# Kernel optimization log

Hardware: AMD Instinct MI355X
Metric: run time of the kernel (lower is better)

The kernel has to match this reference:

```python
import jax, jax.numpy as jnp
import numpy as np

N, H, C = 65536, 256, 512  # tokens, hidden_dim, cond_dim


def setup_inputs() -> dict:
    key = jax.random.key(0)
    ks = jax.random.split(key, 8)
    s_h = 1.0 / np.sqrt(H)
    s_c = 1.0 / np.sqrt(C)
    return {
        "x": jax.random.normal(ks[0], (N, H), dtype=jnp.float32),
        "cond": jax.random.normal(ks[1], (N, C), dtype=jnp.float32),
        # FiLM: Linear(cond_dim -> 2*hidden_dim), output split into (gamma, beta)
        "W_film": jax.random.uniform(ks[2], (C, 2 * H), jnp.float32, -s_c, s_c),
        "b_film": jax.random.uniform(ks[3], (2 * H,), jnp.float32, -s_c, s_c),
        "W1": jax.random.uniform(ks[4], (H, H), jnp.float32, -s_h, s_h),
        "b1": jax.random.uniform(ks[5], (H,), jnp.float32, -s_h, s_h),
        "W2": jax.random.uniform(ks[6], (H, H), jnp.float32, -s_h, s_h),
        "b2": jax.random.uniform(ks[7], (H,), jnp.float32, -s_h, s_h),
    }


def reference(x, cond, W_film, b_film, W1, b1, W2, b2):
    # FiLM conditioning: gamma * x + beta (cond path; LayerNorm branch unused)
    gb = cond @ W_film + b_film            # [N, 2H]
    gamma, beta = gb[:, :H], gb[:, H:]
    h = gamma * x + beta
    # Dropout is identity in eval mode.
    h = jax.nn.relu(h) @ W1 + b1           # [N, H]
    h = jax.nn.relu(h) @ W2 + b2           # [N, H]
    return h + x                            # residual
```

## Files before the change

### kernel.cpp

```cpp
#include <hip/hip_runtime.h>
#include <hip/hip_bf16.h>


typedef __attribute__((ext_vector_type(8))) short bf16x8;
typedef __attribute__((ext_vector_type(4))) float f32x4;

typedef unsigned short ushort_t;
typedef unsigned int uint_t;

__device__ __forceinline__ ushort_t f2bf(float f) {
  union { float f; uint_t u; } v; v.f = f;
  uint_t u = v.u;
  return (ushort_t)((u + 0x7FFFu + ((u >> 16) & 1u)) >> 16);
}
__device__ __forceinline__ float bf2f(ushort_t s) {
  union { uint_t u; float f; } v; v.u = ((uint_t)s) << 16;
  return v.f;
}
__device__ __forceinline__ bf16x8 ldfrag(const ushort_t* p) {
  return *reinterpret_cast<const bf16x8*>(p);
}

__global__ void pack_weights(const float* __restrict__ Wf,
                             const float* __restrict__ W1,
                             const float* __restrict__ W2,
                             ushort_t* __restrict__ p1,
                             ushort_t* __restrict__ pW1,
                             ushort_t* __restrict__ pW2) {
  int u = blockIdx.x * 256 + threadIdx.x;
  if (u < 32768) {
    int lane = u & 63, rest = u >> 6;
    int kt = rest & 15;
    int kb = kt * 32 + (lane >> 4) * 8;
    int col = (rest >> 4) * 16 + (lane & 15);
#pragma unroll
    for (int j = 0; j < 8; ++j)
      p1[(size_t)u * 8 + j] = f2bf(Wf[(size_t)(kb + j) * 512 + col]);
  } else if (u < 40960) {
    int v = u - 32768;
    int lane = v & 63;
    int kt = (v >> 6) & 7;
    int kb = kt * 32 + (lane >> 4) * 8;
    int col = (v >> 9) * 16 + (lane & 15);
#pragma unroll
    for (int j = 0; j < 8; ++j)
      pW1[(size_t)v * 8 + j] = f2bf(W1[(size_t)(kb + j) * 256 + col]);
  } else if (u < 49152) {
    int v = u - 40960;
    int lane = v & 63;
    int kt = (v >> 6) & 7;
    int kb = kt * 32 + (lane >> 4) * 8;
    int col = (v >> 9) * 16 + (lane & 15);
#pragma unroll
    for (int j = 0; j < 8; ++j)
      pW2[(size_t)v * 8 + j] = f2bf(W2[(size_t)(kb + j) * 256 + col]);
  }
}

__global__ __launch_bounds__(256, 2)
void film_fused(const float* __restrict__ x, const float* __restrict__ cond,
                const float* __restrict__ b_film, const float* __restrict__ b1,
                const float* __restrict__ b2,
                const ushort_t* __restrict__ p1, const ushort_t* __restrict__ pW1,
                const ushort_t* __restrict__ pW2, float* __restrict__ out) {
  __shared__ __align__(16) char lds[65536];
  char* hbuf = lds;
  char* xbuf = lds + 32768;
  const int r0 = blockIdx.x * 64;
  const int t = threadIdx.x;
  const int w = t >> 6;
  const int l = t & 63;
  const int l15 = l & 15;
  const int lhi = l >> 4;

#pragma unroll
  for (int it = 0; it < 8; ++it) {
    int u = it * 256 + t;
    int row = u >> 5, k8 = u & 31;
    const float4* cs = reinterpret_cast<const float4*>(cond + (size_t)(r0 + row) * 512 + k8 * 8);
    float4 a = cs[0], b = cs[1];
    const float4* xs = reinterpret_cast<const float4*>(x + (size_t)(r0 + row) * 256 + k8 * 8);
    float4 xa = xs[0], xb = xs[1];
    int byte = row * 512 + k8 * 16;
    byte ^= ((row & 15) << 4);
    union { bf16x8 v; ushort_t s[8]; } hc;
    hc.s[0]=f2bf(a.x); hc.s[1]=f2bf(a.y); hc.s[2]=f2bf(a.z); hc.s[3]=f2bf(a.w);
    hc.s[4]=f2bf(b.x); hc.s[5]=f2bf(b.y); hc.s[6]=f2bf(b.z); hc.s[7]=f2bf(b.w);
    *reinterpret_cast<bf16x8*>(hbuf + byte) = hc.v;
    union { bf16x8 v; ushort_t s[8]; } hx;
    hx.s[0]=f2bf(xa.x); hx.s[1]=f2bf(xa.y); hx.s[2]=f2bf(xa.z); hx.s[3]=f2bf(xa.w);
    hx.s[4]=f2bf(xb.x); hx.s[5]=f2bf(xb.y); hx.s[6]=f2bf(xb.z); hx.s[7]=f2bf(xb.w);
    *reinterpret_cast<bf16x8*>(xbuf + byte) = hx.v;
  }

  bf16x8 bb[2][8];
#pragma unroll
  for (int tt = 0; tt < 8; ++tt) {
    int nt = (tt < 4) ? (w * 4 + tt) : (16 + w * 4 + (tt - 4));
    bb[0][tt] = ldfrag(p1 + ((nt * 16 + 0) * 64 + l) * 8);
  }
  __syncthreads();

  f32x4 acc1[4][8];
#pragma unroll
  for (int m = 0; m < 4; ++m)
#pragma unroll
    for (int n = 0; n < 8; ++n) acc1[m][n] = (f32x4){0.f, 0.f, 0.f, 0.f};

#pragma unroll
  for (int ktg = 0; ktg < 16; ++ktg) {
    if (ktg == 8) {
      __syncthreads();
#pragma unroll
      for (int it = 0; it < 8; ++it) {
        int u = it * 256 + t;
        int row = u >> 5, k8 = u & 31;
        const float4* cs = reinterpret_cast<const float4*>(cond + (size_t)(r0 + row) * 512 + 256 + k8 * 8);
        float4 a = cs[0], b = cs[1];
        int byte = row * 512 + k8 * 16;
        byte ^= ((row & 15) << 4);
        union { bf16x8 v; ushort_t s[8]; } hc;
        hc.s[0]=f2bf(a.x); hc.s[1]=f2bf(a.y); hc.s[2]=f2bf(a.z); hc.s[3]=f2bf(a.w);
        hc.s[4]=f2bf(b.x); hc.s[5]=f2bf(b.y); hc.s[6]=f2bf(b.z); hc.s[7]=f2bf(b.w);
        *reinterpret_cast<bf16x8*>(hbuf + byte) = hc.v;
      }
      __syncthreads();
    }
    const int cur = ktg & 1;
    if (ktg < 15) {
#pragma unroll
      for (int tt = 0; tt < 8; ++tt) {
        int nt = (tt < 4) ? (w * 4 + tt) : (16 + w * 4 + (tt - 4));
        bb[cur ^ 1][tt] = ldfrag(p1 + ((nt * 16 + (ktg + 1)) * 64 + l) * 8);
      }
    }
    bf16x8 afr[4];
    int ktl = ktg & 7;
#pragma unroll
    for (int m = 0; m < 4; ++m) {
      int row = m * 16 + l15;
      int byte = row * 512 + ktl * 64 + lhi * 16;
      byte ^= ((row & 15) << 4);
      afr[m] = *reinterpret_cast<const bf16x8*>(hbuf + byte);
    }
#pragma unroll
    for (int tt = 0; tt < 8; ++tt)
#pragma unroll
      for (int m = 0; m < 4; ++m)
        acc1[m][tt] = __builtin_amdgcn_mfma_f32_16x16x32_bf16(afr[m], bb[cur][tt], acc1[m][tt], 0, 0, 0);
  }
  __syncthreads();

#pragma unroll
  for (int tt = 0; tt < 4; ++tt) {
    int colg = w * 64 + tt * 16 + l15;
    float bg = b_film[colg];
    float bbv = b_film[256 + colg];
#pragma unroll
    for (int m = 0; m < 4; ++m) {
#pragma unroll
      for (int reg = 0; reg < 4; ++reg) {
        int row = m * 16 + lhi * 4 + reg;
        int byte = row * 512 + colg * 2;
        byte ^= ((row & 15) << 4);
        float xv = bf2f(*reinterpret_cast<const ushort_t*>(xbuf + byte));
        float h = fmaxf((acc1[m][tt][reg] + bg) * xv + (acc1[m][4 + tt][reg] + bbv), 0.f);
        *reinterpret_cast<ushort_t*>(hbuf + byte) = f2bf(h);
      }
    }
  }
  bf16x8 bb2[2][4];
#pragma unroll
  for (int tt = 0; tt < 4; ++tt) {
    int nt = w * 4 + tt;
    bb2[0][tt] = ldfrag(pW1 + ((nt * 8 + 0) * 64 + l) * 8);
  }
  __syncthreads();

  f32x4 acc2[4][4];
#pragma unroll
  for (int m = 0; m < 4; ++m)
#pragma unroll
    for (int n = 0; n < 4; ++n) acc2[m][n] = (f32x4){0.f, 0.f, 0.f, 0.f};

#pragma unroll
  for (int kt = 0; kt < 8; ++kt) {
    const int cur = kt & 1;
    if (kt < 7) {
#pragma unroll
      for (int tt = 0; tt < 4; ++tt) {
        int nt = w * 4 + tt;
        bb2[cur ^ 1][tt] = ldfrag(pW1 + ((nt * 8 + (kt + 1)) * 64 + l) * 8);
      }
    }
    bf16x8 afr[4];
#pragma unroll
    for (int m = 0; m < 4; ++m) {
      int row = m * 16 + l15;
      int byte = row * 512 + kt * 64 + lhi * 16;
      byte ^= ((row & 15) << 4);
      afr[m] = *reinterpret_cast<const bf16x8*>(hbuf + byte);
    }
#pragma unroll
    for (int tt = 0; tt < 4; ++tt)
#pragma unroll
      for (int m = 0; m < 4; ++m)
        acc2[m][tt] = __builtin_amdgcn_mfma_f32_16x16x32_bf16(afr[m], bb2[cur][tt], acc2[m][tt], 0, 0, 0);
  }
  __syncthreads();

#pragma unroll
  for (int tt = 0; tt < 4; ++tt) {
    int colg = w * 64 + tt * 16 + l15;
    float bias = b1[colg];
#pragma unroll
    for (int m = 0; m < 4; ++m) {
#pragma unroll
      for (int reg = 0; reg < 4; ++reg) {
        int row = m * 16 + lhi * 4 + reg;
        int byte = row * 512 + colg * 2;
        byte ^= ((row & 15) << 4);
        *reinterpret_cast<ushort_t*>(hbuf + byte) = f2bf(fmaxf(acc2[m][tt][reg] + bias, 0.f));
      }
    }
  }
  bf16x8 bb3[2][4];
#pragma unroll
  for (int tt = 0; tt < 4; ++tt) {
    int nt = w * 4 + tt;
    bb3[0][tt] = ldfrag(pW2 + ((nt * 8 + 0) * 64 + l) * 8);
  }
  __syncthreads();

  f32x4 acc3[4][4];
#pragma unroll
  for (int m = 0; m < 4; ++m)
#pragma unroll
    for (int n = 0; n < 4; ++n) acc3[m][n] = (f32x4){0.f, 0.f, 0.f, 0.f};

#pragma unroll
  for (int kt = 0; kt < 8; ++kt) {
    const int cur = kt & 1;
    if (kt < 7) {
#pragma unroll
      for (int tt = 0; tt < 4; ++tt) {
        int nt = w * 4 + tt;
        bb3[cur ^ 1][tt] = ldfrag(pW2 + ((nt * 8 + (kt + 1)) * 64 + l) * 8);
      }
    }
    bf16x8 afr[4];
#pragma unroll
    for (int m = 0; m < 4; ++m) {
      int row = m * 16 + l15;
      int byte = row * 512 + kt * 64 + lhi * 16;
      byte ^= ((row & 15) << 4);
      afr[m] = *reinterpret_cast<const bf16x8*>(hbuf + byte);
    }
#pragma unroll
    for (int tt = 0; tt < 4; ++tt)
#pragma unroll
      for (int m = 0; m < 4; ++m)
        acc3[m][tt] = __builtin_amdgcn_mfma_f32_16x16x32_bf16(afr[m], bb3[cur][tt], acc3[m][tt], 0, 0, 0);
  }
  __syncthreads();

  float b2v[4];
#pragma unroll
  for (int tt = 0; tt < 4; ++tt) b2v[tt] = b2[w * 64 + tt * 16 + l15];

#pragma unroll
  for (int h = 0; h < 2; ++h) {
#pragma unroll
    for (int tt = 0; tt < 4; ++tt) {
      int colg = w * 64 + tt * 16 + l15;
#pragma unroll
      for (int mm = 0; mm < 2; ++mm) {
        int m = h * 2 + mm;
#pragma unroll
        for (int reg = 0; reg < 4; ++reg) {
          int r = mm * 16 + lhi * 4 + reg;
          int byte = r * 1024 + colg * 4;
          byte ^= ((r & 15) << 4);
          *reinterpret_cast<float*>(hbuf + byte) = acc3[m][tt][reg] + b2v[tt];
        }
      }
    }
    __syncthreads();
#pragma unroll
    for (int i = 0; i < 8; ++i) {
      int u = i * 256 + t;
      int r = u >> 6, c4 = u & 63;
      int byte = r * 1024 + c4 * 16;
      byte ^= ((r & 15) << 4);
      f32x4 v = *reinterpret_cast<const f32x4*>(hbuf + byte);
      int grow = h * 32 + r;
      int xbyte = grow * 512 + c4 * 8;
      xbyte ^= ((grow & 15) << 4);
      const ushort_t* xp = reinterpret_cast<const ushort_t*>(xbuf + xbyte);
      v.x += bf2f(xp[0]); v.y += bf2f(xp[1]); v.z += bf2f(xp[2]); v.w += bf2f(xp[3]);
      f32x4* op = reinterpret_cast<f32x4*>(out + (size_t)(r0 + grow) * 256 + c4 * 4);
      __builtin_nontemporal_store(v, op);
    }
    if (h == 0) __syncthreads();
  }
}

extern "C" void kernel_launch(void* const* d_in, const int* in_sizes, int n_in,
                              void* d_out, int out_size, void* d_ws, size_t ws_size,
                              hipStream_t stream) {
  const float* x      = (const float*)d_in[0];
  const float* cond   = (const float*)d_in[1];
  const float* W_film = (const float*)d_in[2];
  const float* b_film = (const float*)d_in[3];
  const float* W1     = (const float*)d_in[4];
  const float* b1     = (const float*)d_in[5];
  const float* W2     = (const float*)d_in[6];
  const float* b2     = (const float*)d_in[7];
  float* out = (float*)d_out;

  ushort_t* p1  = (ushort_t*)d_ws;
  ushort_t* pW1 = p1 + 262144;
  ushort_t* pW2 = pW1 + 65536;

  hipLaunchKernelGGL(pack_weights, dim3(192), dim3(256), 0, stream,
                     W_film, W1, W2, p1, pW1, pW2);
  hipLaunchKernelGGL(film_fused, dim3(65536 / 64), dim3(256), 0, stream,
                     x, cond, b_film, b1, b2, p1, pW1, pW2, out);
}
```

Before: 108.0 us.

## Load full cond tile upfront, read x from global, double-buffer hidden activations in LDS

Stages the whole 64x512 bf16 cond tile into LDS at once, so the mid-GEMM reload and its two barriers go away. x is no longer kept as bf16 in LDS. The FiLM epilogue reads x straight from global in the MFMA accumulator layout, and the residual re-reads fp32 x with coalesced float4 loads. The second hidden activation goes to a separate LDS half, so the GEMM2 and GEMM3 epilogues need fewer barriers, and all biases are hoisted into registers. This trades extra global reads of x, including strided scalar loads, and more register pressure for less synchronisation and a full-precision residual.

Measured after the change: 141.8 us. 31.3% more time.

```diff
diff --git a/kernel.cpp b/kernel.cpp
--- a/kernel.cpp
+++ b/kernel.cpp
@@ -64,8 +64,7 @@
                 const ushort_t* __restrict__ p1, const ushort_t* __restrict__ pW1,
                 const ushort_t* __restrict__ pW2, float* __restrict__ out) {
   __shared__ __align__(16) char lds[65536];
-  char* hbuf = lds;
-  char* xbuf = lds + 32768;
+  char* r2buf = lds + 32768;
   const int r0 = blockIdx.x * 64;
   const int t = threadIdx.x;
   const int w = t >> 6;
@@ -73,24 +72,28 @@
   const int l15 = l & 15;
   const int lhi = l >> 4;
 
-#pragma unroll
-  for (int it = 0; it < 8; ++it) {
+  float bgv[4], bbv[4], b1v[4], b2v[4];
+#pragma unroll
+  for (int tt = 0; tt < 4; ++tt) {
+    int colg = w * 64 + tt * 16 + l15;
+    bgv[tt] = b_film[colg];
+    bbv[tt] = b_film[256 + colg];
+    b1v[tt] = b1[colg];
+    b2v[tt] = b2[colg];
+  }
+
+#pragma unroll
+  for (int it = 0; it < 16; ++it) {
     int u = it * 256 + t;
-    int row = u >> 5, k8 = u & 31;
+    int row = u >> 6, k8 = u & 63;
     const float4* cs = reinterpret_cast<const float4*>(cond + (size_t)(r0 + row) * 512 + k8 * 8);
     float4 a = cs[0], b = cs[1];
-    const float4* xs = reinterpret_cast<const float4*>(x + (size_t)(r0 + row) * 256 + k8 * 8);
-    float4 xa = xs[0], xb = xs[1];
-    int byte = row * 512 + k8 * 16;
+    int byte = row * 1024 + k8 * 16;
     byte ^= ((row & 15) << 4);
     union { bf16x8 v; ushort_t s[8]; } hc;
     hc.s[0]=f2bf(a.x); hc.s[1]=f2bf(a.y); hc.s[2]=f2bf(a.z); hc.s[3]=f2bf(a.w);
     hc.s[4]=f2bf(b.x); hc.s[5]=f2bf(b.y); hc.s[6]=f2bf(b.z); hc.s[7]=f2bf(b.w);
-    *reinterpret_cast<bf16x8*>(hbuf + byte) = hc.v;
-    union { bf16x8 v; ushort_t s[8]; } hx;
-    hx.s[0]=f2bf(xa.x); hx.s[1]=f2bf(xa.y); hx.s[2]=f2bf(xa.z); hx.s[3]=f2bf(xa.w);
-    hx.s[4]=f2bf(xb.x); hx.s[5]=f2bf(xb.y); hx.s[6]=f2bf(xb.z); hx.s[7]=f2bf(xb.w);
-    *reinterpret_cast<bf16x8*>(xbuf + byte) = hx.v;
+    *reinterpret_cast<bf16x8*>(lds + byte) = hc.v;
   }
 
   bf16x8 bb[2][8];
@@ -109,23 +112,6 @@
 
 #pragma unroll
   for (int ktg = 0; ktg < 16; ++ktg) {
-    if (ktg == 8) {
-      __syncthreads();
-#pragma unroll
-      for (int it = 0; it < 8; ++it) {
-        int u = it * 256 + t;
-        int row = u >> 5, k8 = u & 31;
-        const float4* cs = reinterpret_cast<const float4*>(cond + (size_t)(r0 + row) * 512 + 256 + k8 * 8);
-        float4 a = cs[0], b = cs[1];
-        int byte = row * 512 + k8 * 16;
-        byte ^= ((row & 15) << 4);
-        union { bf16x8 v; ushort_t s[8]; } hc;
-        hc.s[0]=f2bf(a.x); hc.s[1]=f2bf(a.y); hc.s[2]=f2bf(a.z); hc.s[3]=f2bf(a.w);
-        hc.s[4]=f2bf(b.x); hc.s[5]=f2bf(b.y); hc.s[6]=f2bf(b.z); hc.s[7]=f2bf(b.w);
-        *reinterpret_cast<bf16x8*>(hbuf + byte) = hc.v;
-      }
-      __syncthreads();
-    }
     const int cur = ktg & 1;
     if (ktg < 15) {
 #pragma unroll
@@ -135,13 +121,12 @@
       }
     }
     bf16x8 afr[4];
-    int ktl = ktg & 7;
 #pragma unroll
     for (int m = 0; m < 4; ++m) {
       int row = m * 16 + l15;
-      int byte = row * 512 + ktl * 64 + lhi * 16;
+      int byte = row * 1024 + ktg * 64 + lhi * 16;
       byte ^= ((row & 15) << 4);
-      afr[m] = *reinterpret_cast<const bf16x8*>(hbuf + byte);
+      afr[m] = *reinterpret_cast<const bf16x8*>(lds + byte);
     }
 #pragma unroll
     for (int tt = 0; tt < 8; ++tt)
@@ -149,13 +134,87 @@
       for (int m = 0; m < 4; ++m)
         acc1[m][tt] = __builtin_amdgcn_mfma_f32_16x16x32_bf16(afr[m], bb[cur][tt], acc1[m][tt], 0, 0, 0);
   }
-  __syncthreads();
-
+
+  float xv[4][16];
+#pragma unroll
+  for (int m = 0; m < 4; ++m) {
+#pragma unroll
+    for (int tt = 0; tt < 4; ++tt) {
+#pragma unroll
+      for (int reg = 0; reg < 4; ++reg) {
+        int row = m * 16 + lhi * 4 + reg;
+        int colg = w * 64 + tt * 16 + l15;
+        xv[m][tt * 4 + reg] = x[(size_t)(r0 + row) * 256 + colg];
+      }
+    }
+  }
+  bf16x8 bb2[2][4];
+#pragma unroll
+  for (int tt = 0; tt < 4; ++tt) {
+    int nt = w * 4 + tt;
+    bb2[0][tt] = ldfrag(pW1 + ((nt * 8 + 0) * 64 + l) * 8);
+  }
+  __syncthreads();
+
+#pragma unroll
+  for (int m = 0; m < 4; ++m) {
+#pragma unroll
+    for (int tt = 0; tt < 4; ++tt) {
+      int colg = w * 64 + tt * 16 + l15;
+#pragma unroll
+      for (int reg = 0; reg < 4; ++reg) {
+        int row = m * 16 + lhi * 4 + reg;
+        float g = acc1[m][tt][reg] + bgv[tt];
+        float be = acc1[m][4 + tt][reg] + bbv[tt];
+        float h = fmaxf(g * xv[m][tt * 4 + reg] + be, 0.f);
+        int byte = row * 512 + colg * 2;
+        byte ^= ((row & 15) << 4);
+        *reinterpret_cast<ushort_t*>(lds + byte) = f2bf(h);
+      }
+    }
+  }
+  __syncthreads();
+
+  f32x4 acc2[4][4];
+#pragma unroll
+  for (int m = 0; m < 4; ++m)
+#pragma unroll
+    for (int n = 0; n < 4; ++n) acc2[m][n] = (f32x4){0.f, 0.f, 0.f, 0.f};
+
+#pragma unroll
+  for (int kt = 0; kt < 8; ++kt) {
+    const int cur = kt & 1;
+    if (kt < 7) {
+#pragma unroll
+      for (int tt = 0; tt < 4; ++tt) {
+        int nt = w * 4 + tt;
+        bb2[cur ^ 1][tt] = ldfrag(pW1 + ((nt * 8 + (kt + 1)) * 64 + l) * 8);
+      }
+    }
+    bf16x8 afr[4];
+#pragma unroll
+    for (int m = 0; m < 4; ++m) {
+      int row = m * 16 + l15;
+      int byte = row * 512 + kt * 64 + lhi * 16;
+      byte ^= ((row & 15) << 4);
+      afr[m] = *reinterpret_cast<const bf16x8*>(lds + byte);
+    }
+#pragma unroll
+    for (int tt = 0; tt < 4; ++tt)
+#pragma unroll
+      for (int m = 0; m < 4; ++m)
+        acc2[m][tt] = __builtin_amdgcn_mfma_f32_16x16x32_bf16(afr[m], bb2[cur][tt], acc2[m][tt], 0, 0, 0);
+  }
+
+  bf16x8 bb3[2][4];
+#pragma unroll
+  for (int tt = 0; tt < 4; ++tt) {
+    int nt = w * 4 + tt;
+    bb3[0][tt] = ldfrag(pW2 + ((nt * 8 + 0) * 64 + l) * 8);
+  }
 #pragma unroll
   for (int tt = 0; tt < 4; ++tt) {
     int colg = w * 64 + tt * 16 + l15;
-    float bg = b_film[colg];
-    float bbv = b_film[256 + colg];
 #pragma unroll
     for (int m = 0; m < 4; ++m) {
 #pragma unroll
@@ -163,25 +222,17 @@
         int row = m * 16 + lhi * 4 + reg;
         int byte = row * 512 + colg * 2;
         byte ^= ((row & 15) << 4);
-        float xv = bf2f(*reinterpret_cast<const ushort_t*>(xbuf + byte));
-        float h = fmaxf((acc1[m][tt][reg] + bg) * xv + (acc1[m][4 + tt][reg] + bbv), 0.f);
-        *reinterpret_cast<ushort_t*>(hbuf + byte) = f2bf(h);
-      }
-    }
-  }
-  bf16x8 bb2[2][4];
-#pragma unroll
-  for (int tt = 0; tt < 4; ++tt) {
-    int nt = w * 4 + tt;
-    bb2[0][tt] = ldfrag(pW1 + ((nt * 8 + 0) * 64 + l) * 8);
-  }
-  __syncthreads();
-
-  f32x4 acc2[4][4];
+        *reinterpret_cast<ushort_t*>(r2buf + byte) = f2bf(fmaxf(acc2[m][tt][reg] + b1v[tt], 0.f));
+      }
+    }
+  }
+  __syncthreads();
+
+  f32x4 acc3[4][4];
 #pragma unroll
   for (int m = 0; m < 4; ++m)
 #pragma unroll
-    for (int n = 0; n < 4; ++n) acc2[m][n] = (f32x4){0.f, 0.f, 0.f, 0.f};
+    for (int n = 0; n < 4; ++n) acc3[m][n] = (f32x4){0.f, 0.f, 0.f, 0.f};
 
 #pragma unroll
   for (int kt = 0; kt < 8; ++kt) {
@@ -190,7 +241,7 @@
 #pragma unroll
       for (int tt = 0; tt < 4; ++tt) {
         int nt = w * 4 + tt;
-        bb2[cur ^ 1][tt] = ldfrag(pW1 + ((nt * 8 + (kt + 1)) * 64 + l) * 8);
+        bb3[cur ^ 1][tt] = ldfrag(pW2 + ((nt * 8 + (kt + 1)) * 64 + l) * 8);
       }
     }
     bf16x8 afr[4];
@@ -199,109 +250,41 @@
       int row = m * 16 + l15;
       int byte = row * 512 + kt * 64 + lhi * 16;
       byte ^= ((row & 15) << 4);
-      afr[m] = *reinterpret_cast<const bf16x8*>(hbuf + byte);
+      afr[m] = *reinterpret_cast<const bf16x8*>(r2buf + byte);
     }
 #pragma unroll
     for (int tt = 0; tt < 4; ++tt)
 #pragma unroll
       for (int m = 0; m < 4; ++m)
-        acc2[m][tt] = __builtin_amdgcn_mfma_f32_16x16x32_bf16(afr[m], bb2[cur][tt], acc2[m][tt], 0, 0, 0);
+        acc3[m][tt] = __builtin_amdgcn_mfma_f32_16x16x32_bf16(afr[m], bb3[cur][tt], acc3[m][tt], 0, 0, 0);
   }
   __syncthreads();
 
 #pragma unroll
   for (int tt = 0; tt < 4; ++tt) {
     int colg = w * 64 + tt * 16 + l15;
-    float bias = b1[colg];
 #pragma unroll
     for (int m = 0; m < 4; ++m) {
 #pragma unroll
       for (int reg = 0; reg < 4; ++reg) {
         int row = m * 16 + lhi * 4 + reg;
-        int byte = row * 512 + colg * 2;
+        int byte = row * 1024 + colg * 4;
         byte ^= ((row & 15) << 4);
-        *reinterpret_cast<ushort_t*>(hbuf + byte) = f2bf(fmaxf(acc2[m][tt][reg] + bias, 0.f));
-      }
-    }
-  }
-  bf16x8 bb3[2][4];
-#pragma unroll
-  for (int tt = 0; tt < 4; ++tt) {
-    int nt = w * 4 + tt;
-    bb3[0][tt] = ldfrag(pW2 + ((nt * 8 + 0) * 64 + l) * 8);
-  }
-  __syncthreads();
-
-  f32x4 acc3[4][4];
-#pragma unroll
-  for (int m = 0; m < 4; ++m)
-#pragma unroll
-    for (int n = 0; n < 4; ++n) acc3[m][n] = (f32x4){0.f, 0.f, 0.f, 0.f};
-
-#pragma unroll
-  for (int kt = 0; kt < 8; ++kt) {
-    const int cur = kt & 1;
-    if (kt < 7) {
-#pragma unroll
-      for (int tt = 0; tt < 4; ++tt) {
-        int nt = w * 4 + tt;
-        bb3[cur ^ 1][tt] = ldfrag(pW2 + ((nt * 8 + (kt + 1)) * 64 + l) * 8);
-      }
-    }
-    bf16x8 afr[4];
-#pragma unroll
-    for (int m = 0; m < 4; ++m) {
-      int row = m * 16 + l15;
-      int byte = row * 512 + kt * 64 + lhi * 16;
-      byte ^= ((row & 15) << 4);
-      afr[m] = *reinterpret_cast<const bf16x8*>(hbuf + byte);
-    }
-#pragma unroll
-    for (int tt = 0; tt < 4; ++tt)
-#pragma unroll
-      for (int m = 0; m < 4; ++m)
-        acc3[m][tt] = __builtin_amdgcn_mfma_f32_16x16x32_bf16(afr[m], bb3[cur][tt], acc3[m][tt], 0, 0, 0);
-  }
-  __syncthreads();
-
-  float b2v[4];
-#pragma unroll
-  for (int tt = 0; tt < 4; ++tt) b2v[tt] = b2[w * 64 + tt * 16 + l15];
-
-#pragma unroll
-  for (int h = 0; h < 2; ++h) {
-#pragma unroll
-    for (int tt = 0; tt < 4; ++tt) {
-      int colg = w * 64 + tt * 16 + l15;
-#pragma unroll
-      for (int mm = 0; mm < 2; ++mm) {
-        int m = h * 2 + mm;
-#pragma unroll
-        for (int reg = 0; reg < 4; ++reg) {
-          int r = mm * 16 + lhi * 4 + reg;
-          int byte = r * 1024 + colg * 4;
-          byte ^= ((r & 15) << 4);
-          *reinterpret_cast<float*>(hbuf + byte) = acc3[m][tt][reg] + b2v[tt];
-        }
-      }
-    }
-    __syncthreads();
-#pragma unroll
-    for (int i = 0; i < 8; ++i) {
-      int u = i * 256 + t;
-      int r = u >> 6, c4 = u & 63;
-      int byte = r * 1024 + c4 * 16;
-      byte ^= ((r & 15) << 4);
-      f32x4 v = *reinterpret_cast<const f32x4*>(hbuf + byte);
-      int grow = h * 32 + r;
-      int xbyte = grow * 512 + c4 * 8;
-      xbyte ^= ((grow & 15) << 4);
-      const ushort_t* xp = reinterpret_cast<const ushort_t*>(xbuf + xbyte);
-      v.x += bf2f(xp[0]); v.y += bf2f(xp[1]); v.z += bf2f(xp[2]); v.w += bf2f(xp[3]);
-      f32x4* op = reinterpret_cast<f32x4*>(out + (size_t)(r0 + grow) * 256 + c4 * 4);
-      __builtin_nontemporal_store(v, op);
-    }
-    if (h == 0) __syncthreads();
+        *reinterpret_cast<float*>(lds + byte) = acc3[m][tt][reg] + b2v[tt];
+      }
+    }
+  }
+  __syncthreads();
+#pragma unroll
+  for (int i = 0; i < 16; ++i) {
+    int row = i * 4 + w;
+    int byte = row * 1024 + l * 16;
+    byte ^= ((row & 15) << 4);
+    f32x4 v = *reinterpret_cast<const f32x4*>(lds + byte);
+    const float4 xres = *reinterpret_cast<const float4*>(x + (size_t)(r0 + row) * 256 + l * 4);
+    v.x += xres.x; v.y += xres.y; v.z += xres.z; v.w += xres.w;
+    f32x4* op = reinterpret_cast<f32x4*>(out + (size_t)(r0 + row) * 256 + l * 4);
+    __builtin_nontemporal_store(v, op);
   }
 }
 
```
